# Performance work log

Hardware: AMD Instinct MI355X
Metric: run time of the kernel (lower is better)

## Reference

```python
import jax, jax.numpy as jnp
import numpy as np
from jax import lax

L, B, D = 2048, 16, 1024

def setup_inputs() -> dict:
    key = jax.random.key(0)
    k1, k2, k3 = jax.random.split(key, 3)
    prev_layer = jax.random.normal(k1, (L, B, D), dtype=jnp.float32)
    hidden = jax.random.normal(k2, (B, D), dtype=jnp.float32)
    W = jax.random.normal(k3, (3 * D, D), dtype=jnp.float32) * (1.0 / np.sqrt(D))
    b = jnp.zeros((3 * D,), dtype=jnp.float32)
    return {"prev_layer": prev_layer, "hidden": hidden, "W": W, "b": b}

def reference(prev_layer, hidden, W, b):
    # prev_layer: [L, B, D], hidden: [B, D], W: [3D, D], b: [3D]
    d = hidden.shape[-1]
    # nn.Linear: y = x @ W.T + b  (dropout p=0 -> identity)
    preact = jnp.einsum('lbi,oi->lbo', prev_layer, W) + b  # [L, B, 3D]
    x_t = preact[..., :d]                                   # candidate
    gates = jax.nn.sigmoid(preact[..., d:])                 # [L, B, 2D]
    z = gates[..., :d]
    h_gate = gates[..., d:]

    def step(h, zx):
        zt, xt = zx
        s = (1.0 - zt) * h + zt * xt
        return s, s

    hidden_final, ss = lax.scan(step, hidden, (z, x_t))     # ss: [L, B, D]
    out = (1.0 - h_gate) * ss + h_gate * prev_layer         # highway (input_size==output_size)
    return out, hidden_final
```

## Files before the change

kernel.cpp:

```cpp
#include <hip/hip_runtime.h>
#include <cstdint>

#define L_DIM 2048
#define B_DIM 16
#define D_DIM 1024
#define M_DIM (L_DIM*B_DIM)
#define N_DIM (3*D_DIM)
#define K_DIM D_DIM
#define NCH   (B_DIM*D_DIM)
#define SEG   64
#define SEGLEN (L_DIM/SEG)
#define CG    (NCH/8)

#define BK 64
#define NKT (K_DIM/BK)
#define BUF 65536

typedef __bf16 bf16x8 __attribute__((ext_vector_type(8)));
typedef float f32x4 __attribute__((ext_vector_type(4)));

__device__ inline float bf2f(ushort u){ return __uint_as_float(((unsigned)u)<<16); }
__device__ inline ushort f2bf(float f){
  unsigned u = __float_as_uint(f);
  u += 0x7fffu + ((u>>16)&1u);
  return (ushort)(u>>16);
}

__global__ __launch_bounds__(256) void cvt8(const float* __restrict__ in,
                                            ushort* __restrict__ out, int n8){
  int t = blockIdx.x*256 + threadIdx.x;
  if (t >= n8) return;
  const float4* p = (const float4*)(in + (size_t)t*8);
  float4 a = p[0], b = p[1];
  ushort r[8] = {f2bf(a.x),f2bf(a.y),f2bf(a.z),f2bf(a.w),
                 f2bf(b.x),f2bf(b.y),f2bf(b.z),f2bf(b.w)};
  *(uint4*)(out + (size_t)t*8) = *(const uint4*)r;
}

#define GLOAD(gp, lp) __builtin_amdgcn_global_load_lds( \
    (const __attribute__((address_space(1))) void*)(gp), \
    (__attribute__((address_space(3))) void*)(lp), 16, 0, 0)

__global__ __launch_bounds__(1024, 4) void gemm_sru(
    const ushort* __restrict__ gA,
    const ushort* __restrict__ gB,
    const float* __restrict__ bias,
    ushort* __restrict__ xbuf, ushort* __restrict__ zbuf, ushort* __restrict__ hbuf)
{
  __shared__ ulong2 lds_[2*BUF/16];
  char* ldsb = (char*)lds_;

  const int tid  = threadIdx.x;
  const int lane = tid & 63, w = tid >> 6;
  const int wr = (w>>2)*64;
  const int wc = (w&3)*64;

  const int bid = blockIdx.x;
  const int swz = (bid & 7)*192 + (bid >> 3);
  const int bm = (swz / (N_DIM/256))*256, bn = (swz % (N_DIM/256))*256;

  const int l15 = lane & 15, l4 = lane >> 4;
  const int s0 = ((l4)     ^ (l15&7)) * 16;
  const int s1 = ((4 + l4) ^ (l15&7)) * 16;
  const char* pA = ldsb + (wr + l15)*128;
  const char* pB = ldsb + 32768 + (wc + l15)*128;

  const int gsl = (tid & 7) ^ ((tid >> 3) & 7);
  const ushort* gAp = gA + (size_t)(bm + (tid>>3))*K_DIM + gsl*8;
  const ushort* gBp = gB + (size_t)(bn + (tid>>3))*K_DIM + gsl*8;

  f32x4 acc[4][4];
  #pragma unroll
  for (int i=0;i<4;i++)
    #pragma unroll
    for (int j=0;j<4;j++) acc[i][j] = (f32x4){0.f,0.f,0.f,0.f};

#define STAGE(tt) do{ \
    char* d = ldsb + ((tt)&1)*BUF; \
    GLOAD(gAp + (size_t)(tt)*BK,                  d + tid*16); \
    GLOAD(gAp + (size_t)128*K_DIM + (size_t)(tt)*BK, d + 16384 + tid*16); \
    GLOAD(gBp + (size_t)(tt)*BK,                  d + 32768 + tid*16); \
    GLOAD(gBp + (size_t)128*K_DIM + (size_t)(tt)*BK, d + 49152 + tid*16); \
  }while(0)

  STAGE(0);
  __syncthreads();

  for (int t = 0; t < NKT; ++t) {
    const int bo = (t&1)*BUF;
    if (t < NKT-1) STAGE(t+1);

    bf16x8 a0 = *(const bf16x8*)(pA + bo + 0*2048 + s0);
    bf16x8 a1 = *(const bf16x8*)(pA + bo + 1*2048 + s0);
    bf16x8 a2 = *(const bf16x8*)(pA + bo + 2*2048 + s0);
    bf16x8 a3 = *(const bf16x8*)(pA + bo + 3*2048 + s0);
    bf16x8 b0 = *(const bf16x8*)(pB + bo + 0*2048 + s0);
    bf16x8 b1 = *(const bf16x8*)(pB + bo + 1*2048 + s0);
    bf16x8 b2 = *(const bf16x8*)(pB + bo + 2*2048 + s0);
    bf16x8 b3 = *(const bf16x8*)(pB + bo + 3*2048 + s0);
    __builtin_amdgcn_s_setprio(1);
    acc[0][0] = __builtin_amdgcn_mfma_f32_16x16x32_bf16(a0, b0, acc[0][0], 0,0,0);
    acc[0][1] = __builtin_amdgcn_mfma_f32_16x16x32_bf16(a0, b1, acc[0][1], 0,0,0);
    acc[0][2] = __builtin_amdgcn_mfma_f32_16x16x32_bf16(a0, b2, acc[0][2], 0,0,0);
    acc[0][3] = __builtin_amdgcn_mfma_f32_16x16x32_bf16(a0, b3, acc[0][3], 0,0,0);
    acc[1][0] = __builtin_amdgcn_mfma_f32_16x16x32_bf16(a1, b0, acc[1][0], 0,0,0);
    acc[1][1] = __builtin_amdgcn_mfma_f32_16x16x32_bf16(a1, b1, acc[1][1], 0,0,0);
    acc[1][2] = __builtin_amdgcn_mfma_f32_16x16x32_bf16(a1, b2, acc[1][2], 0,0,0);
    acc[1][3] = __builtin_amdgcn_mfma_f32_16x16x32_bf16(a1, b3, acc[1][3], 0,0,0);
    acc[2][0] = __builtin_amdgcn_mfma_f32_16x16x32_bf16(a2, b0, acc[2][0], 0,0,0);
    acc[2][1] = __builtin_amdgcn_mfma_f32_16x16x32_bf16(a2, b1, acc[2][1], 0,0,0);
    acc[2][2] = __builtin_amdgcn_mfma_f32_16x16x32_bf16(a2, b2, acc[2][2], 0,0,0);
    acc[2][3] = __builtin_amdgcn_mfma_f32_16x16x32_bf16(a2, b3, acc[2][3], 0,0,0);
    acc[3][0] = __builtin_amdgcn_mfma_f32_16x16x32_bf16(a3, b0, acc[3][0], 0,0,0);
    acc[3][1] = __builtin_amdgcn_mfma_f32_16x16x32_bf16(a3, b1, acc[3][1], 0,0,0);
    acc[3][2] = __builtin_amdgcn_mfma_f32_16x16x32_bf16(a3, b2, acc[3][2], 0,0,0);
    acc[3][3] = __builtin_amdgcn_mfma_f32_16x16x32_bf16(a3, b3, acc[3][3], 0,0,0);
    __builtin_amdgcn_s_setprio(0);

    a0 = *(const bf16x8*)(pA + bo + 0*2048 + s1);
    a1 = *(const bf16x8*)(pA + bo + 1*2048 + s1);
    a2 = *(const bf16x8*)(pA + bo + 2*2048 + s1);
    a3 = *(const bf16x8*)(pA + bo + 3*2048 + s1);
    b0 = *(const bf16x8*)(pB + bo + 0*2048 + s1);
    b1 = *(const bf16x8*)(pB + bo + 1*2048 + s1);
    b2 = *(const bf16x8*)(pB + bo + 2*2048 + s1);
    b3 = *(const bf16x8*)(pB + bo + 3*2048 + s1);
    __builtin_amdgcn_s_setprio(1);
    acc[0][0] = __builtin_amdgcn_mfma_f32_16x16x32_bf16(a0, b0, acc[0][0], 0,0,0);
    acc[0][1] = __builtin_amdgcn_mfma_f32_16x16x32_bf16(a0, b1, acc[0][1], 0,0,0);
    acc[0][2] = __builtin_amdgcn_mfma_f32_16x16x32_bf16(a0, b2, acc[0][2], 0,0,0);
    acc[0][3] = __builtin_amdgcn_mfma_f32_16x16x32_bf16(a0, b3, acc[0][3], 0,0,0);
    acc[1][0] = __builtin_amdgcn_mfma_f32_16x16x32_bf16(a1, b0, acc[1][0], 0,0,0);
    acc[1][1] = __builtin_amdgcn_mfma_f32_16x16x32_bf16(a1, b1, acc[1][1], 0,0,0);
    acc[1][2] = __builtin_amdgcn_mfma_f32_16x16x32_bf16(a1, b2, acc[1][2], 0,0,0);
    acc[1][3] = __builtin_amdgcn_mfma_f32_16x16x32_bf16(a1, b3, acc[1][3], 0,0,0);
    acc[2][0] = __builtin_amdgcn_mfma_f32_16x16x32_bf16(a2, b0, acc[2][0], 0,0,0);
    acc[2][1] = __builtin_amdgcn_mfma_f32_16x16x32_bf16(a2, b1, acc[2][1], 0,0,0);
    acc[2][2] = __builtin_amdgcn_mfma_f32_16x16x32_bf16(a2, b2, acc[2][2], 0,0,0);
    acc[2][3] = __builtin_amdgcn_mfma_f32_16x16x32_bf16(a2, b3, acc[2][3], 0,0,0);
    acc[3][0] = __builtin_amdgcn_mfma_f32_16x16x32_bf16(a3, b0, acc[3][0], 0,0,0);
    acc[3][1] = __builtin_amdgcn_mfma_f32_16x16x32_bf16(a3, b1, acc[3][1], 0,0,0);
    acc[3][2] = __builtin_amdgcn_mfma_f32_16x16x32_bf16(a3, b2, acc[3][2], 0,0,0);
    acc[3][3] = __builtin_amdgcn_mfma_f32_16x16x32_bf16(a3, b3, acc[3][3], 0,0,0);
    __builtin_amdgcn_s_setprio(0);

    __syncthreads();
  }

  const int region = bn >> 10;
  ushort* dst = region==0 ? xbuf : (region==1 ? zbuf : hbuf);
  ushort* lds16 = (ushort*)ldsb;
  float bv[4];
  #pragma unroll
  for (int g=0; g<4; ++g) bv[g] = bias[bn + wc + g*16 + l15];

  #pragma unroll
  for (int f=0; f<4; ++f)
    #pragma unroll
    for (int g=0; g<4; ++g)
      #pragma unroll
      for (int r=0; r<4; ++r){
        int row = wr + f*16 + l4*4 + r;
        int col = wc + g*16 + l15;
        float v = acc[f][g][r] + bv[g];
        if (region) v = 1.f/(1.f + __expf(-v));
        int slot = col >> 3;
        lds16[row*256 + (((slot ^ (row&31))&31)<<3) + (col&7)] = f2bf(v);
      }
  __syncthreads();
  const int cb = bn & (D_DIM-1);
  #pragma unroll
  for (int i=0;i<8;i++){
    int off = i*16384 + tid*16;
    int row = off >> 9;
    int slot = (off >> 4) & 31;
    int dcol = (off & 511) >> 1;
    const char* src = ldsb + row*512 + (((slot ^ (row&31))&31)<<4);
    *(uint4*)(dst + (size_t)(bm+row)*D_DIM + cb + dcol) = *(const uint4*)src;
  }
#undef STAGE
}

__global__ __launch_bounds__(256) void scan_pass1(
    const ushort* __restrict__ z, const ushort* __restrict__ x,
    float* __restrict__ Aout, float* __restrict__ Bout)
{
  int t = blockIdx.x*256 + threadIdx.x;
  int cg = t & (CG-1), g = t >> 11;
  int c0 = cg*8;
  size_t base = (size_t)g*SEGLEN*NCH + c0;
  float A[8], Bc[8];
  #pragma unroll
  for (int j=0;j<8;j++){ A[j]=1.f; Bc[j]=0.f; }
  #pragma unroll 4
  for (int i=0;i<SEGLEN;i++){
    uint4 zv = *(const uint4*)(z + base + (size_t)i*NCH);
    uint4 xv = *(const uint4*)(x + base + (size_t)i*NCH);
    const ushort* zp = (const ushort*)&zv;
    const ushort* xp = (const ushort*)&xv;
    #pragma unroll
    for (int j=0;j<8;j++){
      float zf = bf2f(zp[j]);
      float a  = 1.f - zf;
      float bb = zf * bf2f(xp[j]);
      Bc[j] = a*Bc[j] + bb;
      A[j]  = a*A[j];
    }
  }
  float* Ao = Aout + (size_t)g*NCH + c0;
  float* Bo = Bout + (size_t)g*NCH + c0;
  *(float4*)Ao     = make_float4(A[0],A[1],A[2],A[3]);
  *(float4*)(Ao+4) = make_float4(A[4],A[5],A[6],A[7]);
  *(float4*)Bo     = make_float4(Bc[0],Bc[1],Bc[2],Bc[3]);
  *(float4*)(Bo+4) = make_float4(Bc[4],Bc[5],Bc[6],Bc[7]);
}

__global__ __launch_bounds__(256) void scan_pass2(
    const float* __restrict__ A, const float* __restrict__ B,
    const float* __restrict__ h0, float* __restrict__ seg, float* __restrict__ hfin)
{
  int c = blockIdx.x*256 + threadIdx.x;
  float s = h0[c];
  #pragma unroll 8
  for (int g=0; g<SEG; g++){
    seg[(size_t)g*NCH + c] = s;
    s = A[(size_t)g*NCH + c]*s + B[(size_t)g*NCH + c];
  }
  hfin[c] = s;
}

__global__ __launch_bounds__(256) void scan_pass3(
    const ushort* __restrict__ z, const ushort* __restrict__ x, const ushort* __restrict__ hg,
    const float* __restrict__ prev, const float* __restrict__ seg,
    float* __restrict__ out)
{
  int t = blockIdx.x*256 + threadIdx.x;
  int cg = t & (CG-1), g = t >> 11;
  int c0 = cg*8;
  float s[8];
  *(float4*)s     = *(const float4*)(seg + (size_t)g*NCH + c0);
  *(float4*)(s+4) = *(const float4*)(seg + (size_t)g*NCH + c0 + 4);
  size_t base = (size_t)g*SEGLEN*NCH + c0;
  #pragma unroll 2
  for (int i=0;i<SEGLEN;i++){
    size_t idx = base + (size_t)i*NCH;
    uint4 zv = *(const uint4*)(z+idx);
    uint4 xv = *(const uint4*)(x+idx);
    uint4 hv = *(const uint4*)(hg+idx);
    float4 p0 = *(const float4*)(prev+idx);
    float4 p1 = *(const float4*)(prev+idx+4);
    const ushort* zp=(const ushort*)&zv;
    const ushort* xp=(const ushort*)&xv;
    const ushort* hp=(const ushort*)&hv;
    float pv[8] = {p0.x,p0.y,p0.z,p0.w,p1.x,p1.y,p1.z,p1.w};
    float o[8];
    #pragma unroll
    for (int j=0;j<8;j++){
      float zf = bf2f(zp[j]);
      s[j] += zf*(bf2f(xp[j]) - s[j]);
      float hf = bf2f(hp[j]);
      o[j] = s[j] + hf*(pv[j] - s[j]);
    }
    *(float4*)(out+idx)   = make_float4(o[0],o[1],o[2],o[3]);
    *(float4*)(out+idx+4) = make_float4(o[4],o[5],o[6],o[7]);
  }
}

extern "C" void kernel_launch(void* const* d_in, const int* in_sizes, int n_in,
                              void* d_out, int out_size, void* d_ws, size_t ws_size,
                              hipStream_t stream) {
  const float* prev = (const float*)d_in[0];
  const float* h0   = (const float*)d_in[1];
  const float* W    = (const float*)d_in[2];
  const float* bias = (const float*)d_in[3];
  float* out  = (float*)d_out;
  float* hfin = out + (size_t)M_DIM*D_DIM;

  char* ws = (char*)d_ws;
  ushort* Ab = (ushort*)ws;
  ushort* Wb = (ushort*)(ws + (size_t)M_DIM*K_DIM*2);
  ushort* xb = (ushort*)(ws + (size_t)M_DIM*K_DIM*2 + (size_t)N_DIM*K_DIM*2);
  ushort* zb = xb + (size_t)M_DIM*D_DIM;
  ushort* hb = zb + (size_t)M_DIM*D_DIM;
  float* Abuf = (float*)ws;
  float* Bbuf = Abuf + (size_t)SEG*NCH;
  float* segb = Bbuf + (size_t)SEG*NCH;

  cvt8<<<(M_DIM*K_DIM/8 + 255)/256, 256, 0, stream>>>(prev, Ab, M_DIM*K_DIM/8);
  cvt8<<<(N_DIM*K_DIM/8 + 255)/256, 256, 0, stream>>>(W,    Wb, N_DIM*K_DIM/8);
  gemm_sru<<<(M_DIM/256)*(N_DIM/256), 1024, 0, stream>>>(Ab, Wb, bias, xb, zb, hb);
  scan_pass1<<<(CG*SEG)/256, 256, 0, stream>>>(zb, xb, Abuf, Bbuf);
  scan_pass2<<<NCH/256, 256, 0, stream>>>(Abuf, Bbuf, h0, segb, hfin);
  scan_pass3<<<(CG*SEG)/256, 256, 0, stream>>>(zb, xb, hb, prev, segb, out);
}
```

Baseline: 391.3 us.

## Switch GEMM to 32x32x16 MFMA with k-slice LDS layout and new block mapping

Replaces the 16x16x32 bf16 MFMA tiles with 32x32x16 MFMA tiles, so each wave issues four larger instructions per k-slice instead of sixteen small ones. The LDS staging layout changes from swizzled row-major to k-slice-major (8-element chunks grouped per k-slice), and the epilogue row/column mapping is updated to match. The XCD-aware block swizzle is rewritten so each XCD gets a contiguous range of M blocks across all N tiles. The new LDS reads are unswizzled with 16-byte row strides, which may cause bank conflicts.

```diff
diff --git a/kernel.cpp b/kernel.cpp
--- a/kernel.cpp
+++ b/kernel.cpp
@@ -17,7 +17,7 @@
 #define BUF 65536
 
 typedef __bf16 bf16x8 __attribute__((ext_vector_type(8)));
-typedef float f32x4 __attribute__((ext_vector_type(4)));
+typedef float f32x16 __attribute__((ext_vector_type(16)));
 
 __device__ inline float bf2f(ushort u){ return __uint_as_float(((unsigned)u)<<16); }
 __device__ inline ushort f2bf(float f){
@@ -54,33 +54,33 @@
   const int lane = tid & 63, w = tid >> 6;
   const int wr = (w>>2)*64;
   const int wc = (w&3)*64;
+  const int l31 = lane & 31, l5 = lane >> 5;
 
   const int bid = blockIdx.x;
-  const int swz = (bid & 7)*192 + (bid >> 3);
-  const int bm = (swz / (N_DIM/256))*256, bn = (swz % (N_DIM/256))*256;
-
-  const int l15 = lane & 15, l4 = lane >> 4;
-  const int s0 = ((l4)     ^ (l15&7)) * 16;
-  const int s1 = ((4 + l4) ^ (l15&7)) * 16;
-  const char* pA = ldsb + (wr + l15)*128;
-  const char* pB = ldsb + 32768 + (wc + l15)*128;
-
-  const int gsl = (tid & 7) ^ ((tid >> 3) & 7);
-  const ushort* gAp = gA + (size_t)(bm + (tid>>3))*K_DIM + gsl*8;
-  const ushort* gBp = gB + (size_t)(bn + (tid>>3))*K_DIM + gsl*8;
-
-  f32x4 acc[4][4];
-  #pragma unroll
-  for (int i=0;i<4;i++)
-    #pragma unroll
-    for (int j=0;j<4;j++) acc[i][j] = (f32x4){0.f,0.f,0.f,0.f};
+  const int xcd = bid & 7, idx = bid >> 3;
+  const int mb = xcd*16 + idx/12, nb = idx % 12;
+  const int bm = mb*256, bn = nb*256;
+
+  const char* pA = ldsb + l5*4096 + (wr + l31)*16;
+  const char* pB = ldsb + 32768 + l5*4096 + (wc + l31)*16;
+
+  const ushort* gAp = gA + (size_t)(bm + (tid & 255))*K_DIM + ((tid>>8)&3)*8;
+  const ushort* gBp = gB + (size_t)(bn + (tid & 255))*K_DIM + ((tid>>8)&3)*8;
+
+  f32x16 acc[2][2];
+  #pragma unroll
+  for (int i=0;i<2;i++)
+    #pragma unroll
+    for (int j=0;j<2;j++)
+      #pragma unroll
+      for (int r=0;r<16;r++) acc[i][j][r] = 0.f;
 
 #define STAGE(tt) do{ \
     char* d = ldsb + ((tt)&1)*BUF; \
-    GLOAD(gAp + (size_t)(tt)*BK,                  d + tid*16); \
-    GLOAD(gAp + (size_t)128*K_DIM + (size_t)(tt)*BK, d + 16384 + tid*16); \
-    GLOAD(gBp + (size_t)(tt)*BK,                  d + 32768 + tid*16); \
-    GLOAD(gBp + (size_t)128*K_DIM + (size_t)(tt)*BK, d + 49152 + tid*16); \
+    GLOAD(gAp + (size_t)(tt)*BK,      d + tid*16);               \
+    GLOAD(gAp + (size_t)(tt)*BK + 32, d + 16384 + tid*16);       \
+    GLOAD(gBp + (size_t)(tt)*BK,      d + 32768 + tid*16); \
+    GLOAD(gBp + (size_t)(tt)*BK + 32, d + 49152 + tid*16); \
   }while(0)
 
   STAGE(0);
@@ -90,79 +90,38 @@
     const int bo = (t&1)*BUF;
     if (t < NKT-1) STAGE(t+1);
 
-    bf16x8 a0 = *(const bf16x8*)(pA + bo + 0*2048 + s0);
-    bf16x8 a1 = *(const bf16x8*)(pA + bo + 1*2048 + s0);
-    bf16x8 a2 = *(const bf16x8*)(pA + bo + 2*2048 + s0);
-    bf16x8 a3 = *(const bf16x8*)(pA + bo + 3*2048 + s0);
-    bf16x8 b0 = *(const bf16x8*)(pB + bo + 0*2048 + s0);
-    bf16x8 b1 = *(const bf16x8*)(pB + bo + 1*2048 + s0);
-    bf16x8 b2 = *(const bf16x8*)(pB + bo + 2*2048 + s0);
-    bf16x8 b3 = *(const bf16x8*)(pB + bo + 3*2048 + s0);
-    __builtin_amdgcn_s_setprio(1);
-    acc[0][0] = __builtin_amdgcn_mfma_f32_16x16x32_bf16(a0, b0, acc[0][0], 0,0,0);
-    acc[0][1] = __builtin_amdgcn_mfma_f32_16x16x32_bf16(a0, b1, acc[0][1], 0,0,0);
-    acc[0][2] = __builtin_amdgcn_mfma_f32_16x16x32_bf16(a0, b2, acc[0][2], 0,0,0);
-    acc[0][3] = __builtin_amdgcn_mfma_f32_16x16x32_bf16(a0, b3, acc[0][3], 0,0,0);
-    acc[1][0] = __builtin_amdgcn_mfma_f32_16x16x32_bf16(a1, b0, acc[1][0], 0,0,0);
-    acc[1][1] = __builtin_amdgcn_mfma_f32_16x16x32_bf16(a1, b1, acc[1][1], 0,0,0);
-    acc[1][2] = __builtin_amdgcn_mfma_f32_16x16x32_bf16(a1, b2, acc[1][2], 0,0,0);
-    acc[1][3] = __builtin_amdgcn_mfma_f32_16x16x32_bf16(a1, b3, acc[1][3], 0,0,0);
-    acc[2][0] = __builtin_amdgcn_mfma_f32_16x16x32_bf16(a2, b0, acc[2][0], 0,0,0);
-    acc[2][1] = __builtin_amdgcn_mfma_f32_16x16x32_bf16(a2, b1, acc[2][1], 0,0,0);
-    acc[2][2] = __builtin_amdgcn_mfma_f32_16x16x32_bf16(a2, b2, acc[2][2], 0,0,0);
-    acc[2][3] = __builtin_amdgcn_mfma_f32_16x16x32_bf16(a2, b3, acc[2][3], 0,0,0);
-    acc[3][0] = __builtin_amdgcn_mfma_f32_16x16x32_bf16(a3, b0, acc[3][0], 0,0,0);
-    acc[3][1] = __builtin_amdgcn_mfma_f32_16x16x32_bf16(a3, b1, acc[3][1], 0,0,0);
-    acc[3][2] = __builtin_amdgcn_mfma_f32_16x16x32_bf16(a3, b2, acc[3][2], 0,0,0);
-    acc[3][3] = __builtin_amdgcn_mfma_f32_16x16x32_bf16(a3, b3, acc[3][3], 0,0,0);
-    __builtin_amdgcn_s_setprio(0);
-
-    a0 = *(const bf16x8*)(pA + bo + 0*2048 + s1);
-    a1 = *(const bf16x8*)(pA + bo + 1*2048 + s1);
-    a2 = *(const bf16x8*)(pA + bo + 2*2048 + s1);
-    a3 = *(const bf16x8*)(pA + bo + 3*2048 + s1);
-    b0 = *(const bf16x8*)(pB + bo + 0*2048 + s1);
-    b1 = *(const bf16x8*)(pB + bo + 1*2048 + s1);
-    b2 = *(const bf16x8*)(pB + bo + 2*2048 + s1);
-    b3 = *(const bf16x8*)(pB + bo + 3*2048 + s1);
-    __builtin_amdgcn_s_setprio(1);
-    acc[0][0] = __builtin_amdgcn_mfma_f32_16x16x32_bf16(a0, b0, acc[0][0], 0,0,0);
-    acc[0][1] = __builtin_amdgcn_mfma_f32_16x16x32_bf16(a0, b1, acc[0][1], 0,0,0);
-    acc[0][2] = __builtin_amdgcn_mfma_f32_16x16x32_bf16(a0, b2, acc[0][2], 0,0,0);
-    acc[0][3] = __builtin_amdgcn_mfma_f32_16x16x32_bf16(a0, b3, acc[0][3], 0,0,0);
-    acc[1][0] = __builtin_amdgcn_mfma_f32_16x16x32_bf16(a1, b0, acc[1][0], 0,0,0);
-    acc[1][1] = __builtin_amdgcn_mfma_f32_16x16x32_bf16(a1, b1, acc[1][1], 0,0,0);
-    acc[1][2] = __builtin_amdgcn_mfma_f32_16x16x32_bf16(a1, b2, acc[1][2], 0,0,0);
-    acc[1][3] = __builtin_amdgcn_mfma_f32_16x16x32_bf16(a1, b3, acc[1][3], 0,0,0);
-    acc[2][0] = __builtin_amdgcn_mfma_f32_16x16x32_bf16(a2, b0, acc[2][0], 0,0,0);
-    acc[2][1] = __builtin_amdgcn_mfma_f32_16x16x32_bf16(a2, b1, acc[2][1], 0,0,0);
-    acc[2][2] = __builtin_amdgcn_mfma_f32_16x16x32_bf16(a2, b2, acc[2][2], 0,0,0);
-    acc[2][3] = __builtin_amdgcn_mfma_f32_16x16x32_bf16(a2, b3, acc[2][3], 0,0,0);
-    acc[3][0] = __builtin_amdgcn_mfma_f32_16x16x32_bf16(a3, b0, acc[3][0], 0,0,0);
-    acc[3][1] = __builtin_amdgcn_mfma_f32_16x16x32_bf16(a3, b1, acc[3][1], 0,0,0);
-    acc[3][2] = __builtin_amdgcn_mfma_f32_16x16x32_bf16(a3, b2, acc[3][2], 0,0,0);
-    acc[3][3] = __builtin_amdgcn_mfma_f32_16x16x32_bf16(a3, b3, acc[3][3], 0,0,0);
-    __builtin_amdgcn_s_setprio(0);
-
+    #pragma unroll
+    for (int ks=0; ks<4; ++ks) {
+      bf16x8 a0 = *(const bf16x8*)(pA + bo + ks*8192);
+      bf16x8 a1 = *(const bf16x8*)(pA + bo + ks*8192 + 512);
+      bf16x8 b0 = *(const bf16x8*)(pB + bo + ks*8192);
+      bf16x8 b1 = *(const bf16x8*)(pB + bo + ks*8192 + 512);
+      __builtin_amdgcn_s_setprio(1);
+      acc[0][0] = __builtin_amdgcn_mfma_f32_32x32x16_bf16(a0, b0, acc[0][0], 0,0,0);
+      acc[0][1] = __builtin_amdgcn_mfma_f32_32x32x16_bf16(a0, b1, acc[0][1], 0,0,0);
+      acc[1][0] = __builtin_amdgcn_mfma_f32_32x32x16_bf16(a1, b0, acc[1][0], 0,0,0);
+      acc[1][1] = __builtin_amdgcn_mfma_f32_32x32x16_bf16(a1, b1, acc[1][1], 0,0,0);
+      __builtin_amdgcn_s_setprio(0);
+    }
     __syncthreads();
   }
 
   const int region = bn >> 10;
   ushort* dst = region==0 ? xbuf : (region==1 ? zbuf : hbuf);
   ushort* lds16 = (ushort*)ldsb;
-  float bv[4];
-  #pragma unroll
-  for (int g=0; g<4; ++g) bv[g] = bias[bn + wc + g*16 + l15];
-
-  #pragma unroll
-  for (int f=0; f<4; ++f)
-    #pragma unroll
-    for (int g=0; g<4; ++g)
+  float bvv[2];
+  bvv[0] = bias[bn + wc + l31];
+  bvv[1] = bias[bn + wc + 32 + l31];
+
+  #pragma unroll
+  for (int fa=0; fa<2; ++fa)
+    #pragma unroll
+    for (int fb=0; fb<2; ++fb)
       #pragma unroll
-      for (int r=0; r<4; ++r){
-        int row = wr + f*16 + l4*4 + r;
-        int col = wc + g*16 + l15;
-        float v = acc[f][g][r] + bv[g];
+      for (int r=0; r<16; ++r){
+        int row = wr + fa*32 + (r&3) + ((r>>2)<<3) + (l5<<2);
+        int col = wc + fb*32 + l31;
+        float v = acc[fa][fb][r] + bvv[fb];
         if (region) v = 1.f/(1.f + __expf(-v));
         int slot = col >> 3;
         lds16[row*256 + (((slot ^ (row&31))&31)<<3) + (col&7)] = f2bf(v);
```

After: 498.4 us. 1.27x slower.
